# Kernel optimization log

Hardware: AMD Instinct MI355X
Metric: run time of the kernel (lower is better)

## Reference

```python
import jax, jax.numpy as jnp
import numpy as np

B, S, E, H = 2, 2048, 768, 12
D = E // H  # head_dim = 64


def setup_inputs() -> dict:
    key = jax.random.key(0)
    ks = jax.random.split(key, 5)
    scale = 1.0 / np.sqrt(E)
    return {
        "x": jax.random.normal(ks[0], (B, S, E), dtype=jnp.float32),
        "Wq": jax.random.normal(ks[1], (E, E), dtype=jnp.float32) * scale,
        "bq": jnp.zeros((E,), dtype=jnp.float32),
        "Wk": jax.random.normal(ks[2], (E, E), dtype=jnp.float32) * scale,
        "bk": jnp.zeros((E,), dtype=jnp.float32),
        "Wv": jax.random.normal(ks[3], (E, E), dtype=jnp.float32) * scale,
        "bv": jnp.zeros((E,), dtype=jnp.float32),
        "Wo": jax.random.normal(ks[4], (E, E), dtype=jnp.float32) * scale,
        "bo": jnp.zeros((E,), dtype=jnp.float32),
    }


def reference(x, Wq, bq, Wk, bk, Wv, bv, Wo, bo):
    # Linear layers (torch nn.Linear: y = x @ W^T + b; here W stored as (E,E), use x @ W + b)
    q = (x @ Wq + bq).reshape(B, S, H, D).transpose(0, 2, 1, 3)  # (B,H,S,D)
    k = (x @ Wk + bk).reshape(B, S, H, D).transpose(0, 2, 1, 3)
    v = (x @ Wv + bv).reshape(B, S, H, D).transpose(0, 2, 1, 3)
    scores = jnp.einsum("bhqd,bhkd->bhqk", q, k) / jnp.sqrt(jnp.float32(D))
    weights = jax.nn.softmax(scores, axis=-1)  # (B,H,S,S) -- explicitly returned
    out = jnp.einsum("bhqk,bhkd->bhqd", weights, v)
    out = out.transpose(0, 2, 1, 3).reshape(B, S, E)
    output = out @ Wo + bo
    return (output, weights)
```

## Files before the change

kernel.cpp:

```cpp
#include <hip/hip_runtime.h>
#include <hip/hip_fp16.h>

#define B_ 2
#define S_ 2048
#define E_ 768
#define H_ 12
#define D_ 64
#define BS_ 4096

typedef _Float16 half8 __attribute__((ext_vector_type(8)));
typedef _Float16 half4 __attribute__((ext_vector_type(4)));
typedef float f32x4 __attribute__((ext_vector_type(4)));

#define EXP_C 0.18033688011112042f

__device__ __forceinline__ f32x4 mfma16(half8 a, half8 b, f32x4 c) {
    return __builtin_amdgcn_mfma_f32_16x16x32_f16(a, b, c, 0, 0, 0);
}

__device__ __forceinline__ void gll16(const void* g, void* s) {
    __builtin_amdgcn_global_load_lds((const __attribute__((address_space(1))) void*)g,
                                     (__attribute__((address_space(3))) void*)s, 16, 0, 0);
}

__global__ void prep_kernel(const float* __restrict__ x,
                            const float* __restrict__ W0, const float* __restrict__ W1,
                            const float* __restrict__ W2, const float* __restrict__ W3,
                            _Float16* __restrict__ Wt, _Float16* __restrict__ xh) {
    int z = blockIdx.z;
    if (z == 4) {
        int n = BS_ * E_;
        int stride = 24 * 24 * 256 * 4;
        for (int i = ((blockIdx.y * 24 + blockIdx.x) * 256 + threadIdx.x) * 4; i < n; i += stride) {
            float4 v = *reinterpret_cast<const float4*>(x + i);
            half4 o;
            o.x = (_Float16)v.x; o.y = (_Float16)v.y; o.z = (_Float16)v.z; o.w = (_Float16)v.w;
            *reinterpret_cast<half4*>(xh + i) = o;
        }
        return;
    }
    __shared__ float tile[32][33];
    const float* W = (z == 0) ? W0 : (z == 1) ? W1 : (z == 2) ? W2 : W3;
    _Float16* dst = Wt + (size_t)z * E_ * E_;
    int out0 = blockIdx.x * 32, in0 = blockIdx.y * 32;
    int tx = threadIdx.x & 31, ty = threadIdx.x >> 5;
    #pragma unroll
    for (int r = ty; r < 32; r += 8) tile[r][tx] = W[(size_t)(in0 + r) * E_ + out0 + tx];
    __syncthreads();
    #pragma unroll
    for (int r = ty; r < 32; r += 8) dst[(size_t)(out0 + r) * E_ + in0 + tx] = (_Float16)tile[tx][r];
}

__global__ __launch_bounds__(256) void qkv_kernel(const _Float16* __restrict__ xh,
                                                  const _Float16* __restrict__ Wt,
                                                  const float* __restrict__ bq, const float* __restrict__ bk,
                                                  const float* __restrict__ bv,
                                                  _Float16* __restrict__ qw, _Float16* __restrict__ kw,
                                                  _Float16* __restrict__ vT) {
    __shared__ __align__(16) _Float16 ldsA[2][128 * 32];
    __shared__ __align__(16) _Float16 ldsB[2][128 * 32];
    int n0 = blockIdx.x * 128;
    int m0 = blockIdx.y * 128;
    int mat = n0 / E_;
    int col0 = n0 - mat * E_;
    int tid = threadIdx.x;
    int lane = tid & 63, wv = tid >> 6;
    int l15 = lane & 15, lhi = lane >> 4;
    int wm = wv >> 1, wn = wv & 1;
    const _Float16* Am = xh + (size_t)m0 * E_;
    const _Float16* Bm = Wt + (size_t)mat * E_ * E_ + (size_t)col0 * E_;

    int srow = wv * 16 + (lane >> 2);
    int sc16 = lane & 3;

    auto stage = [&](int buf, int k0) {
        #pragma unroll
        for (int is = 0; is < 2; ++is) {
            int row = is * 64 + srow;
            int c = (sc16 ^ ((row >> 1) & 3)) << 4;
            gll16((const char*)(Am + (size_t)row * E_ + k0) + c, &ldsA[buf][is * 2048 + wv * 512]);
            gll16((const char*)(Bm + (size_t)row * E_ + k0) + c, &ldsB[buf][is * 2048 + wv * 512]);
        }
    };

    f32x4 acc[4][4];
    #pragma unroll
    for (int mi = 0; mi < 4; ++mi)
        #pragma unroll
        for (int nj = 0; nj < 4; ++nj) acc[mi][nj] = (f32x4){0.f, 0.f, 0.f, 0.f};

    stage(0, 0);
    __syncthreads();
    for (int t = 0; t < E_ / 32; ++t) {
        if (t + 1 < E_ / 32) stage((t + 1) & 1, (t + 1) * 32);
        const _Float16* At = ldsA[t & 1];
        const _Float16* Bt = ldsB[t & 1];
        half8 af[4], bf[4];
        #pragma unroll
        for (int mi = 0; mi < 4; ++mi) {
            int row = wm * 64 + mi * 16 + l15;
            af[mi] = *reinterpret_cast<const half8*>(At + row * 32 + ((lhi ^ ((row >> 1) & 3)) << 3));
        }
        #pragma unroll
        for (int nj = 0; nj < 4; ++nj) {
            int row = wn * 64 + nj * 16 + l15;
            bf[nj] = *reinterpret_cast<const half8*>(Bt + row * 32 + ((lhi ^ ((row >> 1) & 3)) << 3));
        }
        #pragma unroll
        for (int mi = 0; mi < 4; ++mi)
            #pragma unroll
            for (int nj = 0; nj < 4; ++nj) acc[mi][nj] = mfma16(af[mi], bf[nj], acc[mi][nj]);
        __syncthreads();
    }

    const float* bias = (mat == 0) ? bq : (mat == 1) ? bk : bv;
    #pragma unroll
    for (int nj = 0; nj < 4; ++nj) {
        int col = col0 + wn * 64 + nj * 16 + l15;
        int h = col >> 6, d = col & 63;
        float bsv = bias[col];
        #pragma unroll
        for (int mi = 0; mi < 4; ++mi) {
            #pragma unroll
            for (int r = 0; r < 4; ++r) {
                int token = m0 + wm * 64 + mi * 16 + lhi * 4 + r;
                int bb = token >> 11, s = token & (S_ - 1);
                _Float16 val = (_Float16)(acc[mi][nj][r] + bsv);
                if (mat == 0)      qw[(((size_t)bb * H_ + h) * S_ + s) * D_ + d] = val;
                else if (mat == 1) kw[(((size_t)bb * H_ + h) * S_ + s) * D_ + d] = val;
                else               vT[(((size_t)bb * H_ + h) * D_ + d) * S_ + s] = val;
            }
        }
    }
}

__global__ __launch_bounds__(256) void attn_kernel(const _Float16* __restrict__ qw,
                                                   const _Float16* __restrict__ kw,
                                                   const _Float16* __restrict__ vT,
                                                   float* __restrict__ wout,
                                                   _Float16* __restrict__ aout) {
    __shared__ __align__(16) _Float16 ldsK[2][64 * 64];
    __shared__ __align__(16) _Float16 ldsV[2][64 * 64];
    __shared__ __align__(16) _Float16 plds[4][16 * 64];
    int dsp = blockIdx.x;
    int wk = (dsp & 7) * 96 + (dsp >> 3);
    int qt = wk & 31, hb = wk >> 5;
    int h = hb % H_, bb = hb / H_;
    int tid = threadIdx.x;
    int lane = tid & 63, w = tid >> 6;
    int l15 = lane & 15, lhi = lane >> 4;
    int q0 = qt * 64 + 16 * w;
    size_t bh = (size_t)bb * H_ + h;
    const _Float16* qbase = qw + bh * S_ * D_;
    const _Float16* kbase = kw + bh * S_ * D_;
    const _Float16* vbase = vT + bh * D_ * S_;

    int srow = w * 8 + (lane >> 3);
    int sc16 = lane & 7;

    auto stageK = [&](int buf, int kt0) {
        #pragma unroll
        for (int is = 0; is < 2; ++is) {
            int row = is * 32 + srow;
            const char* src = (const char*)(kbase + (size_t)(kt0 + row) * D_) + ((sc16 ^ (row & 7)) << 4);
            gll16(src, &ldsK[buf][is * 2048 + w * 512]);
        }
    };
    auto stageV = [&](int buf, int kt0) {
        #pragma unroll
        for (int is = 0; is < 2; ++is) {
            int row = is * 32 + srow;
            const char* src = (const char*)(vbase + (size_t)row * S_ + kt0) + ((sc16 ^ (row & 7)) << 4);
            gll16(src, &ldsV[buf][is * 2048 + w * 512]);
        }
    };

    half8 qa[2];
    #pragma unroll
    for (int kf = 0; kf < 2; ++kf)
        qa[kf] = *reinterpret_cast<const half8*>(qbase + (size_t)(q0 + l15) * D_ + kf * 32 + lhi * 8);

    float lsum = 0.f;
    f32x4 oacc[4];
    #pragma unroll
    for (int df = 0; df < 4; ++df) oacc[df] = (f32x4){0.f, 0.f, 0.f, 0.f};

    stageK(0, 0);
    stageV(0, 0);
    __syncthreads();
    for (int kt = 0; kt < S_ / 64; ++kt) {
        if (kt + 1 < S_ / 64) { stageK((kt + 1) & 1, (kt + 1) * 64); stageV((kt + 1) & 1, (kt + 1) * 64); }
        const _Float16* Kb = ldsK[kt & 1];
        const _Float16* Vb = ldsV[kt & 1];
        #pragma unroll
        for (int nf = 0; nf < 4; ++nf) {
            f32x4 sacc = (f32x4){0.f, 0.f, 0.f, 0.f};
            int rowk = nf * 16 + l15;
            __builtin_amdgcn_s_setprio(1);
            #pragma unroll
            for (int kf = 0; kf < 2; ++kf) {
                half8 kb = *reinterpret_cast<const half8*>(Kb + rowk * 64 + (((kf * 4 + lhi) ^ (rowk & 7)) << 3));
                sacc = mfma16(kb, qa[kf], sacc);
            }
            __builtin_amdgcn_s_setprio(0);
            half4 pk;
            #pragma unroll
            for (int r = 0; r < 4; ++r) {
                float p = exp2f(sacc[r] * EXP_C);
                lsum += p;
                pk[r] = (_Float16)p;
            }
            int ke = nf * 16 + lhi * 4;
            *reinterpret_cast<half4*>(&plds[w][(l15 << 6) + ((((ke >> 3) ^ (l15 & 7)) << 3) | (ke & 7))]) = pk;
        }
        __builtin_amdgcn_s_setprio(1);
        #pragma unroll
        for (int ks = 0; ks < 2; ++ks) {
            half8 pa = *reinterpret_cast<const half8*>(&plds[w][(l15 << 6) + (((ks * 4 + lhi) ^ (l15 & 7)) << 3)]);
            #pragma unroll
            for (int df = 0; df < 4; ++df) {
                int drow = df * 16 + l15;
                half8 vb = *reinterpret_cast<const half8*>(Vb + drow * 64 + (((ks * 4 + lhi) ^ (drow & 7)) << 3));
                oacc[df] = mfma16(pa, vb, oacc[df]);
            }
        }
        __builtin_amdgcn_s_setprio(0);
        __syncthreads();
    }

    lsum += __shfl_xor(lsum, 16);
    lsum += __shfl_xor(lsum, 32);
    float rs = 1.0f / lsum;

    float rsq[4];
    #pragma unroll
    for (int r = 0; r < 4; ++r) rsq[r] = __shfl(rs, lhi * 4 + r);
    #pragma unroll
    for (int df = 0; df < 4; ++df) {
        #pragma unroll
        for (int r = 0; r < 4; ++r) {
            int token = bb * S_ + q0 + lhi * 4 + r;
            aout[(size_t)token * E_ + h * D_ + df * 16 + l15] = (_Float16)(oacc[df][r] * rsq[r]);
        }
    }

    float* wbase = wout + bh * (size_t)S_ * S_ + (size_t)(q0 + l15) * S_;
    stageK(0, 0);
    __syncthreads();
    for (int kt = 0; kt < S_ / 64; ++kt) {
        if (kt + 1 < S_ / 64) stageK((kt + 1) & 1, (kt + 1) * 64);
        const _Float16* Kb = ldsK[kt & 1];
        #pragma unroll
        for (int nf = 0; nf < 4; ++nf) {
            f32x4 sacc = (f32x4){0.f, 0.f, 0.f, 0.f};
            int rowk = nf * 16 + l15;
            __builtin_amdgcn_s_setprio(1);
            #pragma unroll
            for (int kf = 0; kf < 2; ++kf) {
                half8 kb = *reinterpret_cast<const half8*>(Kb + rowk * 64 + (((kf * 4 + lhi) ^ (rowk & 7)) << 3));
                sacc = mfma16(kb, qa[kf], sacc);
            }
            __builtin_amdgcn_s_setprio(0);
            f32x4 pv;
            #pragma unroll
            for (int r = 0; r < 4; ++r) pv[r] = exp2f(sacc[r] * EXP_C) * rs;
            __builtin_nontemporal_store(pv, reinterpret_cast<f32x4*>(&wbase[kt * 64 + nf * 16 + lhi * 4]));
        }
        __syncthreads();
    }
}

__global__ __launch_bounds__(256) void proj_kernel(const _Float16* __restrict__ ah,
                                                   const _Float16* __restrict__ Wto,
                                                   const float* __restrict__ bo,
                                                   float* __restrict__ out) {
    __shared__ __align__(16) _Float16 ldsA[2][128 * 32];
    __shared__ __align__(16) _Float16 ldsB[2][64 * 32];
    int n0 = blockIdx.x * 64;
    int m0 = blockIdx.y * 128;
    int tid = threadIdx.x;
    int lane = tid & 63, wv = tid >> 6;
    int l15 = lane & 15, lhi = lane >> 4;
    int wm = wv >> 1, wn = wv & 1;
    const _Float16* Am = ah + (size_t)m0 * E_;
    const _Float16* Bm = Wto + (size_t)n0 * E_;

    int srow = wv * 16 + (lane >> 2);
    int sc16 = lane & 3;

    auto stage = [&](int buf, int k0) {
        #pragma unroll
        for (int is = 0; is < 2; ++is) {
            int row = is * 64 + srow;
            int c = (sc16 ^ ((row >> 1) & 3)) << 4;
            gll16((const char*)(Am + (size_t)row * E_ + k0) + c, &ldsA[buf][is * 2048 + wv * 512]);
        }
        {
            int row = srow;
            int c = (sc16 ^ ((row >> 1) & 3)) << 4;
            gll16((const char*)(Bm + (size_t)row * E_ + k0) + c, &ldsB[buf][wv * 512]);
        }
    };

    f32x4 acc[4][2];
    #pragma unroll
    for (int mi = 0; mi < 4; ++mi)
        #pragma unroll
        for (int nj = 0; nj < 2; ++nj) acc[mi][nj] = (f32x4){0.f, 0.f, 0.f, 0.f};

    stage(0, 0);
    __syncthreads();
    for (int t = 0; t < E_ / 32; ++t) {
        if (t + 1 < E_ / 32) stage((t + 1) & 1, (t + 1) * 32);
        const _Float16* At = ldsA[t & 1];
        const _Float16* Bt = ldsB[t & 1];
        half8 af[4], bf[2];
        #pragma unroll
        for (int mi = 0; mi < 4; ++mi) {
            int row = wm * 64 + mi * 16 + l15;
            af[mi] = *reinterpret_cast<const half8*>(At + row * 32 + ((lhi ^ ((row >> 1) & 3)) << 3));
        }
        #pragma unroll
        for (int nj = 0; nj < 2; ++nj) {
            int row = wn * 32 + nj * 16 + l15;
            bf[nj] = *reinterpret_cast<const half8*>(Bt + row * 32 + ((lhi ^ ((row >> 1) & 3)) << 3));
        }
        #pragma unroll
        for (int mi = 0; mi < 4; ++mi)
            #pragma unroll
            for (int nj = 0; nj < 2; ++nj) acc[mi][nj] = mfma16(af[mi], bf[nj], acc[mi][nj]);
        __syncthreads();
    }

    #pragma unroll
    for (int nj = 0; nj < 2; ++nj) {
        int col = n0 + wn * 32 + nj * 16 + l15;
        float bsv = bo[col];
        #pragma unroll
        for (int mi = 0; mi < 4; ++mi) {
            #pragma unroll
            for (int r = 0; r < 4; ++r) {
                int token = m0 + wm * 64 + mi * 16 + lhi * 4 + r;
                __builtin_nontemporal_store(acc[mi][nj][r] + bsv, &out[(size_t)token * E_ + col]);
            }
        }
    }
}

extern "C" void kernel_launch(void* const* d_in, const int* in_sizes, int n_in,
                              void* d_out, int out_size, void* d_ws, size_t ws_size,
                              hipStream_t stream) {
    const float* x  = (const float*)d_in[0];
    const float* Wq = (const float*)d_in[1];
    const float* bq = (const float*)d_in[2];
    const float* Wk = (const float*)d_in[3];
    const float* bk = (const float*)d_in[4];
    const float* Wv = (const float*)d_in[5];
    const float* bv = (const float*)d_in[6];
    const float* Wo = (const float*)d_in[7];
    const float* bo = (const float*)d_in[8];

    char* ws = (char*)d_ws;
    _Float16* xh   = (_Float16*)(ws);
    _Float16* Wt   = (_Float16*)(ws + 6291456);
    _Float16* qw   = (_Float16*)(ws + 11010048);
    _Float16* kw   = (_Float16*)(ws + 17301504);
    _Float16* vT   = (_Float16*)(ws + 23592960);
    _Float16* aout = (_Float16*)(ws + 29884416);
    (void)ws_size; (void)in_sizes; (void)n_in; (void)out_size;

    float* out  = (float*)d_out;
    float* wout = out + (size_t)BS_ * E_;

    prep_kernel<<<dim3(24, 24, 5), dim3(256), 0, stream>>>(x, Wq, Wk, Wv, Wo, Wt, xh);
    qkv_kernel<<<dim3(3 * E_ / 128, BS_ / 128), dim3(256), 0, stream>>>(xh, Wt, bq, bk, bv, qw, kw, vT);
    attn_kernel<<<dim3(768), dim3(256), 0, stream>>>(qw, kw, vT, wout, aout);
    proj_kernel<<<dim3(E_ / 64, BS_ / 128), dim3(256), 0, stream>>>(aout, Wt + (size_t)3 * E_ * E_, bo, out);
}
```

Measured before the change: 237.2 us.

## Read K and V tiles directly from global memory instead of LDS staging

Removes the double-buffered global_load_lds staging of K and V tiles in the attention kernel, along with the per-iteration block barriers. Each wave now loads its MFMA operands straight from global memory, relying on L1/L2 caching because the four waves share the same K/V rows. This eliminates barrier stalls and LDS traffic, frees LDS for higher occupancy, and lets waves run independently. In exchange it gives up the explicit prefetch overlap, repeats global loads across waves, and exposes global load latency directly on the MFMA path.

Result: slower. 381.7 us (+60.9%).

```diff
diff --git a/kernel.cpp b/kernel.cpp
--- a/kernel.cpp
+++ b/kernel.cpp
@@ -139,8 +139,6 @@
                                                    const _Float16* __restrict__ vT,
                                                    float* __restrict__ wout,
                                                    _Float16* __restrict__ aout) {
-    __shared__ __align__(16) _Float16 ldsK[2][64 * 64];
-    __shared__ __align__(16) _Float16 ldsV[2][64 * 64];
     __shared__ __align__(16) _Float16 plds[4][16 * 64];
     int dsp = blockIdx.x;
     int wk = (dsp & 7) * 96 + (dsp >> 3);
@@ -155,26 +153,6 @@
     const _Float16* kbase = kw + bh * S_ * D_;
     const _Float16* vbase = vT + bh * D_ * S_;
 
-    int srow = w * 8 + (lane >> 3);
-    int sc16 = lane & 7;
-
-    auto stageK = [&](int buf, int kt0) {
-        #pragma unroll
-        for (int is = 0; is < 2; ++is) {
-            int row = is * 32 + srow;
-            const char* src = (const char*)(kbase + (size_t)(kt0 + row) * D_) + ((sc16 ^ (row & 7)) << 4);
-            gll16(src, &ldsK[buf][is * 2048 + w * 512]);
-        }
-    };
-    auto stageV = [&](int buf, int kt0) {
-        #pragma unroll
-        for (int is = 0; is < 2; ++is) {
-            int row = is * 32 + srow;
-            const char* src = (const char*)(vbase + (size_t)row * S_ + kt0) + ((sc16 ^ (row & 7)) << 4);
-            gll16(src, &ldsV[buf][is * 2048 + w * 512]);
-        }
-    };
-
     half8 qa[2];
     #pragma unroll
     for (int kf = 0; kf < 2; ++kf)
@@ -185,21 +163,15 @@
     #pragma unroll
     for (int df = 0; df < 4; ++df) oacc[df] = (f32x4){0.f, 0.f, 0.f, 0.f};
 
-    stageK(0, 0);
-    stageV(0, 0);
-    __syncthreads();
     for (int kt = 0; kt < S_ / 64; ++kt) {
-        if (kt + 1 < S_ / 64) { stageK((kt + 1) & 1, (kt + 1) * 64); stageV((kt + 1) & 1, (kt + 1) * 64); }
-        const _Float16* Kb = ldsK[kt & 1];
-        const _Float16* Vb = ldsV[kt & 1];
         #pragma unroll
         for (int nf = 0; nf < 4; ++nf) {
             f32x4 sacc = (f32x4){0.f, 0.f, 0.f, 0.f};
-            int rowk = nf * 16 + l15;
+            int rowk = kt * 64 + nf * 16 + l15;
             __builtin_amdgcn_s_setprio(1);
             #pragma unroll
             for (int kf = 0; kf < 2; ++kf) {
-                half8 kb = *reinterpret_cast<const half8*>(Kb + rowk * 64 + (((kf * 4 + lhi) ^ (rowk & 7)) << 3));
+                half8 kb = *reinterpret_cast<const half8*>(kbase + (size_t)rowk * D_ + kf * 32 + lhi * 8);
                 sacc = mfma16(kb, qa[kf], sacc);
             }
             __builtin_amdgcn_s_setprio(0);
@@ -220,12 +192,11 @@
             #pragma unroll
             for (int df = 0; df < 4; ++df) {
                 int drow = df * 16 + l15;
-                half8 vb = *reinterpret_cast<const half8*>(Vb + drow * 64 + (((ks * 4 + lhi) ^ (drow & 7)) << 3));
+                half8 vb = *reinterpret_cast<const half8*>(vbase + (size_t)drow * S_ + kt * 64 + ks * 32 + lhi * 8);
                 oacc[df] = mfma16(pa, vb, oacc[df]);
             }
         }
         __builtin_amdgcn_s_setprio(0);
-        __syncthreads();
     }
 
     lsum += __shfl_xor(lsum, 16);
@@ -245,19 +216,15 @@
     }
 
     float* wbase = wout + bh * (size_t)S_ * S_ + (size_t)(q0 + l15) * S_;
-    stageK(0, 0);
-    __syncthreads();
     for (int kt = 0; kt < S_ / 64; ++kt) {
-        if (kt + 1 < S_ / 64) stageK((kt + 1) & 1, (kt + 1) * 64);
-        const _Float16* Kb = ldsK[kt & 1];
         #pragma unroll
         for (int nf = 0; nf < 4; ++nf) {
             f32x4 sacc = (f32x4){0.f, 0.f, 0.f, 0.f};
-            int rowk = nf * 16 + l15;
+            int rowk = kt * 64 + nf * 16 + l15;
             __builtin_amdgcn_s_setprio(1);
             #pragma unroll
             for (int kf = 0; kf < 2; ++kf) {
-                half8 kb = *reinterpret_cast<const half8*>(Kb + rowk * 64 + (((kf * 4 + lhi) ^ (rowk & 7)) << 3));
+                half8 kb = *reinterpret_cast<const half8*>(kbase + (size_t)rowk * D_ + kf * 32 + lhi * 8);
                 sacc = mfma16(kb, qa[kf], sacc);
             }
             __builtin_amdgcn_s_setprio(0);
@@ -266,7 +233,6 @@
             for (int r = 0; r < 4; ++r) pv[r] = exp2f(sacc[r] * EXP_C) * rs;
             __builtin_nontemporal_store(pv, reinterpret_cast<f32x4*>(&wbase[kt * 64 + nf * 16 + lhi * 4]));
         }
-        __syncthreads();
     }
 }
 
```
